# Optimization experiments

Hardware: AMD Instinct MI355X
Metric: run time of the kernel (lower is better)

Reference implementation:

```python
import jax, jax.numpy as jnp
import numpy as np
import itertools

DIM_X, DIM_Y = 3, 3
MAX_DIGIT = DIM_X * DIM_Y          # 9
NUM_NODES = MAX_DIGIT ** 2         # 81
EMBED = 16
HID = 96
BATCH = 256
ITERS = 4


def determine_edges(dim_x, dim_y):
    md = dim_x * dim_y
    rows = []
    for r in range(md):
        for c in range(md):
            s = {(r, i) for i in range(md)} | {(i, c) for i in range(md)}
            xm, ym = r // dim_x * dim_x, c // dim_y * dim_y
            s |= set(itertools.product(range(xm, xm + dim_x), range(ym, ym + dim_y)))
            s -= {(r, c)}
            rows.append(sorted(i * md + j for i, j in s))
    return np.asarray(rows, dtype=np.int32)  # [81, 20]


def mlp3(x, w0, b0, w1, b1, w2, b2):
    # MLP([a,b,c,d]): two ReLU hidden layers, linear output
    x = jax.nn.relu(x @ w0.T + b0)
    x = jax.nn.relu(x @ w1.T + b1)
    return x @ w2.T + b2


def setup_inputs() -> dict:
    key = jax.random.key(0)
    keys = iter(jax.random.split(key, 40))

    def lin(din, dout):
        kw, kb = jax.random.split(next(keys))
        lim = 1.0 / np.sqrt(din)
        w = jax.random.uniform(kw, (dout, din), jnp.float32, -lim, lim)
        b = jax.random.uniform(kb, (dout,), jnp.float32, -lim, lim)
        return w, b

    embed = jax.random.normal(next(keys), (MAX_DIGIT + 1, EMBED), jnp.float32)

    in_w0, in_b0 = lin(EMBED, HID); in_w1, in_b1 = lin(HID, HID); in_w2, in_b2 = lin(HID, HID)
    f_w0, f_b0 = lin(2 * HID, HID); f_w1, f_b1 = lin(HID, HID); f_w2, f_b2 = lin(HID, HID)
    g_w0, g_b0 = lin(2 * HID, HID); g_w1, g_b1 = lin(HID, HID); g_w2, g_b2 = lin(HID, HID)
    r_w0, r_b0 = lin(HID, HID); r_w1, r_b1 = lin(HID, HID); r_w2, r_b2 = lin(HID, MAX_DIGIT)

    lim = 1.0 / np.sqrt(HID)
    lstm_wih = jax.random.uniform(next(keys), (4 * HID, HID), jnp.float32, -lim, lim)
    lstm_whh = jax.random.uniform(next(keys), (4 * HID, HID), jnp.float32, -lim, lim)
    lstm_bih = jax.random.uniform(next(keys), (4 * HID,), jnp.float32, -lim, lim)
    lstm_bhh = jax.random.uniform(next(keys), (4 * HID,), jnp.float32, -lim, lim)

    grids = jax.random.randint(next(keys), (BATCH, NUM_NODES), 0, MAX_DIGIT + 1)
    c0 = jax.random.normal(next(keys), (BATCH * NUM_NODES, HID), jnp.float32)
    edges = jnp.asarray(determine_edges(DIM_X, DIM_Y))

    return dict(embed=embed,
                in_w0=in_w0, in_b0=in_b0, in_w1=in_w1, in_b1=in_b1, in_w2=in_w2, in_b2=in_b2,
                f_w0=f_w0, f_b0=f_b0, f_w1=f_w1, f_b1=f_b1, f_w2=f_w2, f_b2=f_b2,
                g_w0=g_w0, g_b0=g_b0, g_w1=g_w1, g_b1=g_b1, g_w2=g_w2, g_b2=g_b2,
                lstm_wih=lstm_wih, lstm_whh=lstm_whh, lstm_bih=lstm_bih, lstm_bhh=lstm_bhh,
                r_w0=r_w0, r_b0=r_b0, r_w1=r_w1, r_b1=r_b1, r_w2=r_w2, r_b2=r_b2,
                c0=c0, grids=grids, edges=edges, iters=ITERS)


def reference(embed,
              in_w0, in_b0, in_w1, in_b1, in_w2, in_b2,
              f_w0, f_b0, f_w1, f_b1, f_w2, f_b2,
              g_w0, g_b0, g_w1, g_b1, g_w2, g_b2,
              lstm_wih, lstm_whh, lstm_bih, lstm_bhh,
              r_w0, r_b0, r_w1, r_b1, r_w2, r_b2,
              c0, grids, edges, iters):
    B, N = grids.shape
    K = edges.shape[1]
    emb = embed[grids]                                   # [B, N, EMBED]
    X = mlp3(emb, in_w0, in_b0, in_w1, in_b1, in_w2, in_b2)  # [B, N, HID]
    H = X
    h = X.reshape(B * N, HID)
    c = c0
    outputs = []
    for _ in range(iters):
        # gather neighbor states: [B, N, K, HID]
        Hn = H[:, edges]
        Hs = jnp.broadcast_to(H[:, :, None, :], Hn.shape)
        pair = jnp.concatenate([Hs, Hn], axis=-1)        # [B, N, K, 2*HID]
        M = mlp3(pair, f_w0, f_b0, f_w1, f_b1, f_w2, f_b2).sum(axis=2)  # [B, N, HID]
        gin = mlp3(jnp.concatenate([X, M], axis=-1),
                   g_w0, g_b0, g_w1, g_b1, g_w2, g_b2).reshape(B * N, HID)
        # single-step LSTM (torch gate order: i, f, g, o)
        gates = gin @ lstm_wih.T + lstm_bih + h @ lstm_whh.T + lstm_bhh
        gi, gf, gg, go = jnp.split(gates, 4, axis=-1)
        c = jax.nn.sigmoid(gf) * c + jax.nn.sigmoid(gi) * jnp.tanh(gg)
        h = jax.nn.sigmoid(go) * jnp.tanh(c)
        H = h.reshape(B, N, HID)
        outputs.append(mlp3(H, r_w0, r_b0, r_w1, r_b1, r_w2, r_b2))  # [B, N, MAX_DIGIT]
    return jnp.stack(outputs)  # [iters, B, N, MAX_DIGIT]
```

## Files before the change

### kernel.cpp

```cpp
#include <hip/hip_runtime.h>
#include <hip/hip_bf16.h>

typedef __hip_bfloat16 bf16;
typedef __attribute__((ext_vector_type(8))) short short8;
typedef __attribute__((ext_vector_type(8))) __bf16 bf16x8;
typedef __attribute__((ext_vector_type(4))) float f32x4;

#define BN 20736
#define NNODE 81
#define KNB 20

__device__ inline float bf2f(short s) {
  union { unsigned u; float f; } x; x.u = ((unsigned)(unsigned short)s) << 16; return x.f;
}
__device__ inline short f2bf(float f) {
  __hip_bfloat16 h = __float2bfloat16(f);
  return *reinterpret_cast<short*>(&h);
}
__device__ inline bf16x8 ld8(const bf16* p) {
  return __builtin_bit_cast(bf16x8, *(const short8*)p);
}

__device__ inline void zacc3(f32x4 acc[3]) {
  #pragma unroll
  for (int nt = 0; nt < 3; ++nt) acc[nt] = (f32x4){0.f, 0.f, 0.f, 0.f};
}
__device__ inline void load_w48(const bf16* __restrict__ W, int ldw, int n0, int lr, int lq,
                                bf16x8 wf[3][3]) {
  #pragma unroll
  for (int nt = 0; nt < 3; ++nt)
    #pragma unroll
    for (int ks = 0; ks < 3; ++ks)
      wf[nt][ks] = ld8(&W[(size_t)(n0 + nt * 16 + lr) * ldw + ks * 32 + lq * 8]);
}
__device__ inline void gemm48(const bf16x8 af[3], const bf16x8 wf[3][3], f32x4 acc[3]) {
  #pragma unroll
  for (int ks = 0; ks < 3; ++ks)
    #pragma unroll
    for (int nt = 0; nt < 3; ++nt)
      acc[nt] = __builtin_amdgcn_mfma_f32_16x16x32_bf16(af[ks], wf[nt][ks], acc[nt], 0, 0, 0);
}
__device__ inline void acc_store_cs(float* xw, const f32x4 acc[3], int lr, int lq, int n0) {
  #pragma unroll
  for (int nt = 0; nt < 3; ++nt)
    #pragma unroll
    for (int r = 0; r < 4; ++r)
      xw[(lq * 4 + r) * 100 + n0 + nt * 16 + lr] = acc[nt][r];
}
__device__ inline void xbuf_frag(const float* xw, int lr, int lq,
                                 const float* __restrict__ bias, float bscale,
                                 const bf16* residRow, int act,
                                 bf16x8 af[3]) {
  #pragma unroll
  for (int ks = 0; ks < 3; ++ks) {
    const int c0 = ks * 32 + lq * 8;
    float4 x0 = *(const float4*)&xw[lr * 100 + c0];
    float4 x1 = *(const float4*)&xw[lr * 100 + c0 + 4];
    float xv[8] = {x0.x, x0.y, x0.z, x0.w, x1.x, x1.y, x1.z, x1.w};
    if (bias) {
      float4 b0 = *(const float4*)&bias[c0];
      float4 b1 = *(const float4*)&bias[c0 + 4];
      float bv[8] = {b0.x, b0.y, b0.z, b0.w, b1.x, b1.y, b1.z, b1.w};
      #pragma unroll
      for (int j = 0; j < 8; ++j) xv[j] += bscale * bv[j];
    }
    if (residRow) {
      short8 r8 = *(const short8*)&residRow[c0];
      #pragma unroll
      for (int j = 0; j < 8; ++j) xv[j] += bf2f(r8[j]);
    }
    short8 o;
    #pragma unroll
    for (int j = 0; j < 8; ++j) {
      float v = xv[j];
      if (act) v = fmaxf(v, 0.f);
      o[j] = f2bf(v);
    }
    af[ks] = __builtin_bit_cast(bf16x8, o);
  }
}
__device__ inline void store_frag(bf16* dst, int lq, const bf16x8 af[3]) {
  #pragma unroll
  for (int ks = 0; ks < 3; ++ks)
    *(short8*)&dst[ks * 32 + lq * 8] = __builtin_bit_cast(short8, af[ks]);
}

__global__ __launch_bounds__(256) void prep_k(
    const float* in_w1, const float* in_w2, const float* f_w1, const float* f_w2,
    const float* g_w1, const float* g_w2, const float* r_w0, const float* r_w1,
    const float* r_w2, const float* wih, const float* whh, const float* g_w0,
    const float* f_w0, const float* in_w0, const float* f_b0,
    bf16* inw1b, bf16* inw2b, bf16* fw1b, bf16* fw2b,
    bf16* gw1b, bf16* gw2b, bf16* rw0b, bf16* rw1b,
    bf16* rw2b, bf16* wihb, bf16* whhb, bf16* gw0b,
    bf16* wfnb, bf16* w0pb, float* bias_fn)
{
  int idx = blockIdx.x * 256 + threadIdx.x;
  int y = blockIdx.y;
  const float* src = nullptr; bf16* dst = nullptr; int cnt = 0;
  switch (y) {
    case 0:  src = in_w1; dst = inw1b; cnt = 9216;  break;
    case 1:  src = in_w2; dst = inw2b; cnt = 9216;  break;
    case 2:  src = f_w1;  dst = fw1b;  cnt = 9216;  break;
    case 3:  src = f_w2;  dst = fw2b;  cnt = 9216;  break;
    case 4:  src = g_w1;  dst = gw1b;  cnt = 9216;  break;
    case 5:  src = g_w2;  dst = gw2b;  cnt = 9216;  break;
    case 6:  src = r_w0;  dst = rw0b;  cnt = 9216;  break;
    case 7:  src = r_w1;  dst = rw1b;  cnt = 9216;  break;
    case 8:  src = r_w2;  dst = rw2b;  cnt = 864;   break;
    case 9:  src = wih;   dst = wihb;  cnt = 36864; break;
    case 10: src = whh;   dst = whhb;  cnt = 36864; break;
    case 11: src = g_w0;  dst = gw0b;  cnt = 18432; break;
    case 12: {
      if (idx < 18432) {
        int n = idx / 96, k = idx - n * 96;
        float v = (n < 96) ? f_w0[n * 192 + k] : f_w0[(n - 96) * 192 + 96 + k];
        wfnb[idx] = __float2bfloat16(v);
      }
      return;
    }
    case 13: {
      if (idx < 3072) {
        int n = idx >> 5, k = idx & 31;
        w0pb[idx] = __float2bfloat16(k < 16 ? in_w0[n * 16 + k] : 0.f);
      }
      return;
    }
    default: {
      if (idx < 192) bias_fn[idx] = (idx < 96) ? f_b0[idx] : 0.f;
      return;
    }
  }
  if (idx < cnt) dst[idx] = __float2bfloat16(src[idx]);
}

__global__ __launch_bounds__(256) void fused_in_k(
    const float* __restrict__ embed, const int* __restrict__ grids,
    const bf16* __restrict__ w0pb, const float* __restrict__ in_b0,
    const bf16* __restrict__ inw1b, const float* __restrict__ in_b1,
    const bf16* __restrict__ inw2b, const float* __restrict__ in_b2,
    const bf16* __restrict__ gw0b, const float* __restrict__ g_b0,
    const bf16* __restrict__ wfnb, const float* __restrict__ bias_fn,
    bf16* __restrict__ X, bf16* __restrict__ Xg, bf16* __restrict__ P)
{
  __shared__ float xbuf[2][2][1600];
  const int t = threadIdx.x, w = t >> 6, lane = t & 63, lr = lane & 15, lq = lane >> 4;
  const int mh = w >> 1, ch = w & 1, n0 = ch * 48;
  const int m0 = blockIdx.x * 32 + mh * 16;
  float* x0 = xbuf[0][mh];
  float* x1 = xbuf[1][mh];
  bf16x8 wf[3][3]; f32x4 acc[3]; bf16x8 af[3];

  short8 es = {0, 0, 0, 0, 0, 0, 0, 0};
  if (lq < 2) {
    int gidx = grids[m0 + lr];
    float4 e0 = *(const float4*)&embed[gidx * 16 + lq * 8];
    float4 e1 = *(const float4*)&embed[gidx * 16 + lq * 8 + 4];
    es[0] = f2bf(e0.x); es[1] = f2bf(e0.y); es[2] = f2bf(e0.z); es[3] = f2bf(e0.w);
    es[4] = f2bf(e1.x); es[5] = f2bf(e1.y); es[6] = f2bf(e1.z); es[7] = f2bf(e1.w);
  }
  bf16x8 a0 = __builtin_bit_cast(bf16x8, es);
  #pragma unroll
  for (int nt = 0; nt < 3; ++nt)
    wf[nt][0] = ld8(&w0pb[(size_t)(n0 + nt * 16 + lr) * 32 + lq * 8]);
  zacc3(acc);
  #pragma unroll
  for (int nt = 0; nt < 3; ++nt)
    acc[nt] = __builtin_amdgcn_mfma_f32_16x16x32_bf16(a0, wf[nt][0], acc[nt], 0, 0, 0);
  acc_store_cs(x0, acc, lr, lq, n0);
  __syncthreads();
  xbuf_frag(x0, lr, lq, in_b0, 1.f, nullptr, 1, af);
  load_w48(inw1b, 96, n0, lr, lq, wf); zacc3(acc); gemm48(af, wf, acc);
  acc_store_cs(x1, acc, lr, lq, n0);
  __syncthreads();
  xbuf_frag(x1, lr, lq, in_b1, 1.f, nullptr, 1, af);
  load_w48(inw2b, 96, n0, lr, lq, wf); zacc3(acc); gemm48(af, wf, acc);
  acc_store_cs(x0, acc, lr, lq, n0);
  __syncthreads();
  bf16x8 xf[3];
  xbuf_frag(x0, lr, lq, in_b2, 1.f, nullptr, 0, xf);
  if (ch == 0) store_frag(&X[(size_t)(m0 + lr) * 96], lq, xf);
  load_w48(gw0b, 192, n0, lr, lq, wf); zacc3(acc); gemm48(xf, wf, acc);
  acc_store_cs(x1, acc, lr, lq, n0);
  __syncthreads();
  xbuf_frag(x1, lr, lq, g_b0, 1.f, nullptr, 0, af);
  if (ch == 0) store_frag(&Xg[(size_t)(m0 + lr) * 96], lq, af);
  #pragma unroll
  for (int ph = 0; ph < 2; ++ph) {
    float* xb = ph ? x1 : x0;
    load_w48(wfnb + (size_t)ph * 96 * 96, 96, n0, lr, lq, wf); zacc3(acc); gemm48(xf, wf, acc);
    acc_store_cs(xb, acc, lr, lq, n0);
    __syncthreads();
    xbuf_frag(xb, lr, lq, bias_fn + ph * 96, 1.f, nullptr, 0, af);
    if (ch == 0) store_frag(&P[(size_t)(m0 + lr) * 192 + ph * 96], lq, af);
  }
}

__global__ __launch_bounds__(128) void edge_k(
    const bf16* __restrict__ P, const bf16* __restrict__ w1bf,
    const float* __restrict__ b1, const int* __restrict__ edges,
    const bf16* __restrict__ fw2b, const float* __restrict__ f_b2,
    bf16* __restrict__ M)
{
  __shared__ short zs[80 * 104];
  __shared__ short sbuf[16 * 104];
  const int t = threadIdx.x;
  const int grp = (blockIdx.x & 7) * 648 + (blockIdx.x >> 3);
  const int w = t >> 6, lane = t & 63, lr = lane & 15, lq = lane >> 4;
  const int n0 = w * 48;

  bf16x8 wf1[3][3];
  #pragma unroll
  for (int nt = 0; nt < 3; ++nt)
    #pragma unroll
    for (int ks = 0; ks < 3; ++ks)
      wf1[nt][ks] = ld8(&w1bf[(size_t)(n0 + nt * 16 + lr) * 96 + ks * 32 + lq * 8]);
  float b1v[3];
  #pragma unroll
  for (int nt = 0; nt < 3; ++nt) b1v[nt] = b1[n0 + nt * 16 + lr];

  for (int i = t; i < 12 * 104; i += 128) sbuf[(4 + i / 104) * 104 + (i % 104)] = 0;
  for (int cc = t; cc < 80 * 12; cc += 128) {
    int row = cc / 12, c8 = cc - row * 12;
    int p = row / 20, j = row - p * 20;
    int gr = grp * 4 + p;
    int b = gr / NNODE, i = gr - b * NNODE;
    int e = edges[i * KNB + j];
    short8 a8 = *(const short8*)&P[(size_t)gr * 192 + c8 * 8];
    short8 n8 = *(const short8*)&P[((size_t)b * NNODE + e) * 192 + 96 + c8 * 8];
    short8 z;
    #pragma unroll
    for (int q = 0; q < 8; ++q)
      z[q] = f2bf(fmaxf(bf2f(a8[q]) + bf2f(n8[q]), 0.f));
    *(short8*)&zs[row * 104 + c8 * 8] = z;
  }
  __syncthreads();

  f32x4 acc[5][3];
  #pragma unroll
  for (int mt = 0; mt < 5; ++mt)
    #pragma unroll
    for (int nt = 0; nt < 3; ++nt) acc[mt][nt] = (f32x4){0.f, 0.f, 0.f, 0.f};
  #pragma unroll
  for (int ks = 0; ks < 3; ++ks) {
    const int koff = ks * 32 + lq * 8;
    #pragma unroll
    for (int mt = 0; mt < 5; ++mt) {
      bf16x8 af = __builtin_bit_cast(bf16x8, *(const short8*)&zs[(mt * 16 + lr) * 104 + koff]);
      #pragma unroll
      for (int nt = 0; nt < 3; ++nt)
        acc[mt][nt] = __builtin_amdgcn_mfma_f32_16x16x32_bf16(af, wf1[nt][ks], acc[mt][nt], 0, 0, 0);
    }
  }

  float nodeacc[4][3];
  #pragma unroll
  for (int pp = 0; pp < 4; ++pp)
    #pragma unroll
    for (int nt = 0; nt < 3; ++nt) nodeacc[pp][nt] = 0.f;
  #pragma unroll
  for (int mt = 0; mt < 5; ++mt)
    #pragma unroll
    for (int nt = 0; nt < 3; ++nt)
      #pragma unroll
      for (int r = 0; r < 4; ++r) {
        int row = mt * 16 + lq * 4 + r;
        int p = row / 20;
        float v = fmaxf(acc[mt][nt][r] + b1v[nt], 0.f);
        #pragma unroll
        for (int pp = 0; pp < 4; ++pp)
          nodeacc[pp][nt] += (p == pp) ? v : 0.f;
      }
  #pragma unroll
  for (int pp = 0; pp < 4; ++pp)
    #pragma unroll
    for (int nt = 0; nt < 3; ++nt) {
      float v = nodeacc[pp][nt];
      v += __shfl_xor(v, 16, 64);
      v += __shfl_xor(v, 32, 64);
      if (lq == 0)
        sbuf[pp * 104 + n0 + nt * 16 + lr] = f2bf(v);
    }
  __syncthreads();

  bf16x8 mwf[3][3];
  #pragma unroll
  for (int nt = 0; nt < 3; ++nt)
    #pragma unroll
    for (int ks = 0; ks < 3; ++ks)
      mwf[nt][ks] = ld8(&fw2b[(size_t)(n0 + nt * 16 + lr) * 96 + ks * 32 + lq * 8]);
  f32x4 macc[3];
  zacc3(macc);
  #pragma unroll
  for (int ks = 0; ks < 3; ++ks) {
    bf16x8 af = __builtin_bit_cast(bf16x8, *(const short8*)&sbuf[lr * 104 + ks * 32 + lq * 8]);
    #pragma unroll
    for (int nt = 0; nt < 3; ++nt)
      macc[nt] = __builtin_amdgcn_mfma_f32_16x16x32_bf16(af, mwf[nt][ks], macc[nt], 0, 0, 0);
  }
  if (lq == 0) {
    #pragma unroll
    for (int nt = 0; nt < 3; ++nt) {
      int col = n0 + nt * 16 + lr;
      float bb = (float)KNB * f_b2[col];
      #pragma unroll
      for (int r = 0; r < 4; ++r)
        M[(size_t)(grp * 4 + r) * 96 + col] = __float2bfloat16(macc[nt][r] + bb);
    }
  }
}

__global__ __launch_bounds__(128) void fused_iter_k(
    const bf16* __restrict__ Min,
    const bf16* __restrict__ gw0b, const bf16* __restrict__ Xg,
    const bf16* __restrict__ gw1b, const float* __restrict__ g_b1,
    const bf16* __restrict__ gw2b, const float* __restrict__ g_b2,
    const bf16* __restrict__ Hin,
    const bf16* __restrict__ wihb, const bf16* __restrict__ whhb,
    const float* __restrict__ bih, const float* __restrict__ bhh,
    float* __restrict__ c, bf16* __restrict__ Hout,
    const bf16* __restrict__ wfnb, const float* __restrict__ bias_fn, bf16* __restrict__ P,
    const bf16* __restrict__ rw0b, const float* __restrict__ r_b0,
    const bf16* __restrict__ rw1b, const float* __restrict__ r_b1,
    const bf16* __restrict__ rw2b, const float* __restrict__ r_b2,
    float* __restrict__ outp, int doP)
{
  __shared__ float xb0[1600], xb1[1600];
  const int t = threadIdx.x, w = t >> 6, lane = t & 63, lr = lane & 15, lq = lane >> 4;
  const int n0 = w * 48;
  const int m0 = blockIdx.x * 16;

  bf16x8 wfA[3][3], wfB[3][3], af[3];
  f32x4 acc[3];

  #pragma unroll
  for (int ks = 0; ks < 3; ++ks)
    af[ks] = ld8(&Min[(size_t)(m0 + lr) * 96 + ks * 32 + lq * 8]);
  bf16x8 hin[3];
  #pragma unroll
  for (int ks = 0; ks < 3; ++ks)
    hin[ks] = ld8(&Hin[(size_t)(m0 + lr) * 96 + ks * 32 + lq * 8]);

  load_w48(gw0b + 96, 192, n0, lr, lq, wfA);
  zacc3(acc); gemm48(af, wfA, acc);
  load_w48(gw1b, 96, n0, lr, lq, wfB);
  acc_store_cs(xb0, acc, lr, lq, n0);
  __syncthreads();
  xbuf_frag(xb0, lr, lq, nullptr, 0.f, &Xg[(size_t)(m0 + lr) * 96], 1, af);
  zacc3(acc); gemm48(af, wfB, acc);
  load_w48(gw2b, 96, n0, lr, lq, wfA);
  acc_store_cs(xb1, acc, lr, lq, n0);
  __syncthreads();
  xbuf_frag(xb1, lr, lq, g_b1, 1.f, nullptr, 1, af);
  zacc3(acc); gemm48(af, wfA, acc);
  acc_store_cs(xb0, acc, lr, lq, n0);
  __syncthreads();
  bf16x8 gf[3];
  xbuf_frag(xb0, lr, lq, g_b2, 1.f, nullptr, 0, gf);

  float cv[3][4];
  #pragma unroll
  for (int nt = 0; nt < 3; ++nt)
    #pragma unroll
    for (int r = 0; r < 4; ++r)
      cv[nt][r] = c[(size_t)(m0 + lq * 4 + r) * 96 + n0 + nt * 16 + lr];

  f32x4 ga[4][3];
  #pragma unroll
  for (int g4 = 0; g4 < 4; ++g4)
    #pragma unroll
    for (int nt = 0; nt < 3; ++nt) ga[g4][nt] = (f32x4){0.f, 0.f, 0.f, 0.f};
  #pragma unroll
  for (int g4 = 0; g4 < 4; ++g4)
    #pragma unroll
    for (int nt = 0; nt < 3; ++nt) {
      size_t nrow = (size_t)(g4 * 96 + n0 + nt * 16 + lr) * 96;
      #pragma unroll
      for (int ks = 0; ks < 3; ++ks) {
        ga[g4][nt] = __builtin_amdgcn_mfma_f32_16x16x32_bf16(
            gf[ks], ld8(&wihb[nrow + ks * 32 + lq * 8]), ga[g4][nt], 0, 0, 0);
        ga[g4][nt] = __builtin_amdgcn_mfma_f32_16x16x32_bf16(
            hin[ks], ld8(&whhb[nrow + ks * 32 + lq * 8]), ga[g4][nt], 0, 0, 0);
      }
    }
  #pragma unroll
  for (int nt = 0; nt < 3; ++nt) {
    int col = n0 + nt * 16 + lr;
    float bvi = bih[col] + bhh[col];
    float bvf = bih[96 + col] + bhh[96 + col];
    float bvg = bih[192 + col] + bhh[192 + col];
    float bvo = bih[288 + col] + bhh[288 + col];
    #pragma unroll
    for (int r = 0; r < 4; ++r) {
      int m = m0 + lq * 4 + r;
      size_t idx = (size_t)m * 96 + col;
      float gi = ga[0][nt][r] + bvi;
      float gfv = ga[1][nt][r] + bvf;
      float gg = ga[2][nt][r] + bvg;
      float go = ga[3][nt][r] + bvo;
      float si = 1.f / (1.f + expf(-gi));
      float sf = 1.f / (1.f + expf(-gfv));
      float so = 1.f / (1.f + expf(-go));
      float tg = tanhf(gg);
      float cn = sf * cv[nt][r] + si * tg;
      if (doP) c[idx] = cn;
      xb1[(lq * 4 + r) * 100 + col] = so * tanhf(cn);
    }
  }
  __syncthreads();
  bf16x8 hf[3];
  xbuf_frag(xb1, lr, lq, nullptr, 0.f, nullptr, 0, hf);

  if (doP) {
    for (int cc = t; cc < 192; cc += 128) {
      int row = cc / 12, c8 = cc - row * 12;
      short8 o;
      #pragma unroll
      for (int j = 0; j < 8; ++j) o[j] = f2bf(xb1[row * 100 + c8 * 8 + j]);
      *(short8*)&Hout[(size_t)(m0 + row) * 96 + c8 * 8] = o;
    }
    load_w48(wfnb, 96, n0, lr, lq, wfA);
    zacc3(acc); gemm48(hf, wfA, acc);
    load_w48(wfnb + 96 * 96, 96, n0, lr, lq, wfB);
    #pragma unroll
    for (int nt = 0; nt < 3; ++nt) {
      float bvv = bias_fn[n0 + nt * 16 + lr];
      #pragma unroll
      for (int r = 0; r < 4; ++r)
        xb0[(lq * 4 + r) * 100 + n0 + nt * 16 + lr] = acc[nt][r] + bvv;
    }
    __syncthreads();
    for (int cc = t; cc < 192; cc += 128) {
      int row = cc / 12, c8 = cc - row * 12;
      short8 o;
      #pragma unroll
      for (int j = 0; j < 8; ++j) o[j] = f2bf(xb0[row * 100 + c8 * 8 + j]);
      *(short8*)&P[(size_t)(m0 + row) * 192 + c8 * 8] = o;
    }
    zacc3(acc); gemm48(hf, wfB, acc);
    #pragma unroll
    for (int nt = 0; nt < 3; ++nt) {
      float bvv = bias_fn[96 + n0 + nt * 16 + lr];
      #pragma unroll
      for (int r = 0; r < 4; ++r)
        xb1[(lq * 4 + r) * 100 + n0 + nt * 16 + lr] = acc[nt][r] + bvv;
    }
    __syncthreads();
    for (int cc = t; cc < 192; cc += 128) {
      int row = cc / 12, c8 = cc - row * 12;
      short8 o;
      #pragma unroll
      for (int j = 0; j < 8; ++j) o[j] = f2bf(xb1[row * 100 + c8 * 8 + j]);
      *(short8*)&P[(size_t)(m0 + row) * 192 + 96 + c8 * 8] = o;
    }
  }

  load_w48(rw0b, 96, n0, lr, lq, wfA);
  zacc3(acc); gemm48(hf, wfA, acc);
  load_w48(rw1b, 96, n0, lr, lq, wfB);
  __syncthreads();
  acc_store_cs(xb0, acc, lr, lq, n0);
  __syncthreads();
  xbuf_frag(xb0, lr, lq, r_b0, 1.f, nullptr, 1, af);
  zacc3(acc); gemm48(af, wfB, acc);
  acc_store_cs(xb1, acc, lr, lq, n0);
  __syncthreads();
  xbuf_frag(xb1, lr, lq, r_b1, 1.f, nullptr, 1, af);
  if (w == 0) {
    bf16x8 w9[3];
    #pragma unroll
    for (int ks = 0; ks < 3; ++ks) {
      short8 s = {0, 0, 0, 0, 0, 0, 0, 0};
      if (lr < 9) s = *(const short8*)&rw2b[(size_t)lr * 96 + ks * 32 + lq * 8];
      w9[ks] = __builtin_bit_cast(bf16x8, s);
    }
    f32x4 a9 = (f32x4){0.f, 0.f, 0.f, 0.f};
    #pragma unroll
    for (int ks = 0; ks < 3; ++ks)
      a9 = __builtin_amdgcn_mfma_f32_16x16x32_bf16(af[ks], w9[ks], a9, 0, 0, 0);
    if (lr < 9) {
      float bb = r_b2[lr];
      #pragma unroll
      for (int r = 0; r < 4; ++r)
        outp[(size_t)(m0 + lq * 4 + r) * 9 + lr] = a9[r] + bb;
    }
  }
}

extern "C" void kernel_launch(void* const* d_in, const int* in_sizes, int n_in,
                              void* d_out, int out_size, void* d_ws, size_t ws_size,
                              hipStream_t stream) {
  const float* embed   = (const float*)d_in[0];
  const float* in_w0   = (const float*)d_in[1];
  const float* in_b0   = (const float*)d_in[2];
  const float* in_w1   = (const float*)d_in[3];
  const float* in_b1   = (const float*)d_in[4];
  const float* in_w2   = (const float*)d_in[5];
  const float* in_b2   = (const float*)d_in[6];
  const float* f_w0    = (const float*)d_in[7];
  const float* f_b0    = (const float*)d_in[8];
  const float* f_w1    = (const float*)d_in[9];
  const float* f_b1    = (const float*)d_in[10];
  const float* f_w2    = (const float*)d_in[11];
  const float* f_b2    = (const float*)d_in[12];
  const float* g_w0    = (const float*)d_in[13];
  const float* g_b0    = (const float*)d_in[14];
  const float* g_w1    = (const float*)d_in[15];
  const float* g_b1    = (const float*)d_in[16];
  const float* g_w2    = (const float*)d_in[17];
  const float* g_b2    = (const float*)d_in[18];
  const float* wih     = (const float*)d_in[19];
  const float* whh     = (const float*)d_in[20];
  const float* bih     = (const float*)d_in[21];
  const float* bhh     = (const float*)d_in[22];
  const float* r_w0    = (const float*)d_in[23];
  const float* r_b0    = (const float*)d_in[24];
  const float* r_w1    = (const float*)d_in[25];
  const float* r_b1    = (const float*)d_in[26];
  const float* r_w2    = (const float*)d_in[27];
  const float* r_b2    = (const float*)d_in[28];
  const float* c0      = (const float*)d_in[29];
  const int*   grids   = (const int*)d_in[30];
  const int*   edges   = (const int*)d_in[31];

  float* out = (float*)d_out;
  const int iters = out_size / (BN * 9);

  float* c    = (float*)d_ws;
  bf16* H0    = (bf16*)(c + (size_t)BN * 96);
  bf16* H1    = H0 + (size_t)BN * 96;
  bf16* Xg    = H1 + (size_t)BN * 96;
  bf16* P     = Xg + (size_t)BN * 96;
  bf16* Mb    = P  + (size_t)BN * 192;
  bf16* w0pb  = Mb + (size_t)BN * 96;
  bf16* wfnb  = w0pb + 3072;
  bf16* inw1b = wfnb + 18432;
  bf16* inw2b = inw1b + 9216;
  bf16* fw1b  = inw2b + 9216;
  bf16* fw2b  = fw1b + 9216;
  bf16* gw0b  = fw2b + 9216;
  bf16* gw1b  = gw0b + 18432;
  bf16* gw2b  = gw1b + 9216;
  bf16* rw0b  = gw2b + 9216;
  bf16* rw1b  = rw0b + 9216;
  bf16* rw2b  = rw1b + 9216;
  bf16* wihb  = rw2b + 864;
  bf16* whhb  = wihb + 36864;
  float* bias_fn = (float*)(whhb + 36864);

  prep_k<<<dim3(144, 15), 256, 0, stream>>>(
      in_w1, in_w2, f_w1, f_w2, g_w1, g_w2, r_w0, r_w1, r_w2, wih, whh, g_w0,
      f_w0, in_w0, f_b0,
      inw1b, inw2b, fw1b, fw2b, gw1b, gw2b, rw0b, rw1b, rw2b, wihb, whhb, gw0b,
      wfnb, w0pb, bias_fn);
  fused_in_k<<<BN / 32, 256, 0, stream>>>(embed, grids, w0pb, in_b0, inw1b, in_b1,
                                          inw2b, in_b2, gw0b, g_b0, wfnb, bias_fn,
                                          H0, Xg, P);
  hipMemcpyAsync(c, c0, (size_t)BN * 96 * sizeof(float), hipMemcpyDeviceToDevice, stream);

  for (int it = 0; it < iters; ++it) {
    bf16* Hin  = (it & 1) ? H1 : H0;
    bf16* Hout = (it & 1) ? H0 : H1;
    edge_k<<<BN / 4, 128, 0, stream>>>(P, fw1b, f_b1, edges, fw2b, f_b2, Mb);
    fused_iter_k<<<BN / 16, 128, 0, stream>>>(
        Mb, gw0b, Xg, gw1b, g_b1, gw2b, g_b2,
        Hin, wihb, whhb, bih, bhh, c, Hout,
        wfnb, bias_fn, P, rw0b, r_b0, rw1b, r_b1, rw2b, r_b2,
        out + (size_t)it * BN * 9, it < iters - 1 ? 1 : 0);
  }
}
```

Baseline: 327.6 us.

## Run fused_iter_k with one wavefront per block covering all 96 columns

The per-node iteration kernel now uses a single 64-lane wave per 16-row tile instead of two waves each owning 48 output columns. Each wave computes all 96 columns, with weight fragments streamed straight from global memory inside a new gemm96w helper. This lets every __syncthreads be dropped, since LDS staging is now private to one wave. The trade-off is twice the accumulator registers per wave (the LSTM gate accumulators grow to 4x6 tiles), which may cost occupancy or cause spills, and weights are no longer preloaded ahead of each GEMM.

```diff
diff --git a/kernel.cpp b/kernel.cpp
--- a/kernel.cpp
+++ b/kernel.cpp
@@ -46,6 +46,27 @@
     #pragma unroll
     for (int r = 0; r < 4; ++r)
       xw[(lq * 4 + r) * 100 + n0 + nt * 16 + lr] = acc[nt][r];
+}
+__device__ inline void zacc6(f32x4 acc[6]) {
+  #pragma unroll
+  for (int nt = 0; nt < 6; ++nt) acc[nt] = (f32x4){0.f, 0.f, 0.f, 0.f};
+}
+__device__ inline void gemm96w(const bf16* __restrict__ W, int ldw,
+                               const bf16x8 af[3], int lr, int lq, f32x4 acc[6]) {
+  #pragma unroll
+  for (int nt = 0; nt < 6; ++nt)
+    #pragma unroll
+    for (int ks = 0; ks < 3; ++ks) {
+      bf16x8 wf = ld8(&W[(size_t)(nt * 16 + lr) * ldw + ks * 32 + lq * 8]);
+      acc[nt] = __builtin_amdgcn_mfma_f32_16x16x32_bf16(af[ks], wf, acc[nt], 0, 0, 0);
+    }
+}
+__device__ inline void acc_store96(float* xw, const f32x4 acc[6], int lr, int lq) {
+  #pragma unroll
+  for (int nt = 0; nt < 6; ++nt)
+    #pragma unroll
+    for (int r = 0; r < 4; ++r)
+      xw[(lq * 4 + r) * 100 + nt * 16 + lr] = acc[nt][r];
 }
 __device__ inline void xbuf_frag(const float* xw, int lr, int lq,
                                  const float* __restrict__ bias, float bscale,
@@ -310,7 +331,7 @@
   }
 }
 
-__global__ __launch_bounds__(128) void fused_iter_k(
+__global__ __launch_bounds__(64) void fused_iter_k(
     const bf16* __restrict__ Min,
     const bf16* __restrict__ gw0b, const bf16* __restrict__ Xg,
     const bf16* __restrict__ gw1b, const float* __restrict__ g_b1,
@@ -326,12 +347,11 @@
     float* __restrict__ outp, int doP)
 {
   __shared__ float xb0[1600], xb1[1600];
-  const int t = threadIdx.x, w = t >> 6, lane = t & 63, lr = lane & 15, lq = lane >> 4;
-  const int n0 = w * 48;
+  const int t = threadIdx.x, lr = t & 15, lq = t >> 4;
   const int m0 = blockIdx.x * 16;
 
-  bf16x8 wfA[3][3], wfB[3][3], af[3];
-  f32x4 acc[3];
+  bf16x8 af[3];
+  f32x4 acc[6];
 
   #pragma unroll
   for (int ks = 0; ks < 3; ++ks)
@@ -341,40 +361,34 @@
   for (int ks = 0; ks < 3; ++ks)
     hin[ks] = ld8(&Hin[(size_t)(m0 + lr) * 96 + ks * 32 + lq * 8]);
 
-  load_w48(gw0b + 96, 192, n0, lr, lq, wfA);
-  zacc3(acc); gemm48(af, wfA, acc);
-  load_w48(gw1b, 96, n0, lr, lq, wfB);
-  acc_store_cs(xb0, acc, lr, lq, n0);
-  __syncthreads();
+  zacc6(acc); gemm96w(gw0b + 96, 192, af, lr, lq, acc);
+  acc_store96(xb0, acc, lr, lq);
   xbuf_frag(xb0, lr, lq, nullptr, 0.f, &Xg[(size_t)(m0 + lr) * 96], 1, af);
-  zacc3(acc); gemm48(af, wfB, acc);
-  load_w48(gw2b, 96, n0, lr, lq, wfA);
-  acc_store_cs(xb1, acc, lr, lq, n0);
-  __syncthreads();
+  zacc6(acc); gemm96w(gw1b, 96, af, lr, lq, acc);
+  acc_store96(xb1, acc, lr, lq);
   xbuf_frag(xb1, lr, lq, g_b1, 1.f, nullptr, 1, af);
-  zacc3(acc); gemm48(af, wfA, acc);
-  acc_store_cs(xb0, acc, lr, lq, n0);
-  __syncthreads();
+  zacc6(acc); gemm96w(gw2b, 96, af, lr, lq, acc);
+  acc_store96(xb0, acc, lr, lq);
   bf16x8 gf[3];
   xbuf_frag(xb0, lr, lq, g_b2, 1.f, nullptr, 0, gf);
 
-  float cv[3][4];
-  #pragma unroll
-  for (int nt = 0; nt < 3; ++nt)
+  float cv[6][4];
+  #pragma unroll
+  for (int nt = 0; nt < 6; ++nt)
     #pragma unroll
     for (int r = 0; r < 4; ++r)
-      cv[nt][r] = c[(size_t)(m0 + lq * 4 + r) * 96 + n0 + nt * 16 + lr];
-
-  f32x4 ga[4][3];
+      cv[nt][r] = c[(size_t)(m0 + lq * 4 + r) * 96 + nt * 16 + lr];
+
+  f32x4 ga[4][6];
   #pragma unroll
   for (int g4 = 0; g4 < 4; ++g4)
     #pragma unroll
-    for (int nt = 0; nt < 3; ++nt) ga[g4][nt] = (f32x4){0.f, 0.f, 0.f, 0.f};
+    for (int nt = 0; nt < 6; ++nt) ga[g4][nt] = (f32x4){0.f, 0.f, 0.f, 0.f};
   #pragma unroll
   for (int g4 = 0; g4 < 4; ++g4)
     #pragma unroll
-    for (int nt = 0; nt < 3; ++nt) {
-      size_t nrow = (size_t)(g4 * 96 + n0 + nt * 16 + lr) * 96;
+    for (int nt = 0; nt < 6; ++nt) {
+      size_t nrow = (size_t)(g4 * 96 + nt * 16 + lr) * 96;
       #pragma unroll
       for (int ks = 0; ks < 3; ++ks) {
         ga[g4][nt] = __builtin_amdgcn_mfma_f32_16x16x32_bf16(
@@ -384,8 +398,8 @@
       }
     }
   #pragma unroll
-  for (int nt = 0; nt < 3; ++nt) {
-    int col = n0 + nt * 16 + lr;
+  for (int nt = 0; nt < 6; ++nt) {
+    int col = nt * 16 + lr;
     float bvi = bih[col] + bhh[col];
     float bvf = bih[96 + col] + bhh[96 + col];
     float bvg = bih[192 + col] + bhh[192 + col];
@@ -407,47 +421,48 @@
       xb1[(lq * 4 + r) * 100 + col] = so * tanhf(cn);
     }
   }
-  __syncthreads();
   bf16x8 hf[3];
   xbuf_frag(xb1, lr, lq, nullptr, 0.f, nullptr, 0, hf);
 
   if (doP) {
-    for (int cc = t; cc < 192; cc += 128) {
-      int row = cc / 12, c8 = cc - row * 12;
+    #pragma unroll
+    for (int cc = 0; cc < 3; ++cc) {
+      int idx = t + cc * 64;
+      int row = idx / 12, c8 = idx - row * 12;
       short8 o;
       #pragma unroll
       for (int j = 0; j < 8; ++j) o[j] = f2bf(xb1[row * 100 + c8 * 8 + j]);
       *(short8*)&Hout[(size_t)(m0 + row) * 96 + c8 * 8] = o;
     }
-    load_w48(wfnb, 96, n0, lr, lq, wfA);
-    zacc3(acc); gemm48(hf, wfA, acc);
-    load_w48(wfnb + 96 * 96, 96, n0, lr, lq, wfB);
-    #pragma unroll
-    for (int nt = 0; nt < 3; ++nt) {
-      float bvv = bias_fn[n0 + nt * 16 + lr];
+    zacc6(acc); gemm96w(wfnb, 96, hf, lr, lq, acc);
+    #pragma unroll
+    for (int nt = 0; nt < 6; ++nt) {
+      float bvv = bias_fn[nt * 16 + lr];
       #pragma unroll
       for (int r = 0; r < 4; ++r)
-        xb0[(lq * 4 + r) * 100 + n0 + nt * 16 + lr] = acc[nt][r] + bvv;
-    }
-    __syncthreads();
-    for (int cc = t; cc < 192; cc += 128) {
-      int row = cc / 12, c8 = cc - row * 12;
+        xb0[(lq * 4 + r) * 100 + nt * 16 + lr] = acc[nt][r] + bvv;
+    }
+    #pragma unroll
+    for (int cc = 0; cc < 3; ++cc) {
+      int idx = t + cc * 64;
+      int row = idx / 12, c8 = idx - row * 12;
       short8 o;
       #pragma unroll
       for (int j = 0; j < 8; ++j) o[j] = f2bf(xb0[row * 100 + c8 * 8 + j]);
       *(short8*)&P[(size_t)(m0 + row) * 192 + c8 * 8] = o;
     }
-    zacc3(acc); gemm48(hf, wfB, acc);
-    #pragma unroll
-    for (int nt = 0; nt < 3; ++nt) {
-      float bvv = bias_fn[96 + n0 + nt * 16 + lr];
+    zacc6(acc); gemm96w(wfnb + 96 * 96, 96, hf, lr, lq, acc);
+    #pragma unroll
+    for (int nt = 0; nt < 6; ++nt) {
+      float bvv = bias_fn[96 + nt * 16 + lr];
       #pragma unroll
       for (int r = 0; r < 4; ++r)
-        xb1[(lq * 4 + r) * 100 + n0 + nt * 16 + lr] = acc[nt][r] + bvv;
-    }
-    __syncthreads();
-    for (int cc = t; cc < 192; cc += 128) {
-      int row = cc / 12, c8 = cc - row * 12;
+        xb1[(lq * 4 + r) * 100 + nt * 16 + lr] = acc[nt][r] + bvv;
+    }
+    #pragma unroll
+    for (int cc = 0; cc < 3; ++cc) {
+      int idx = t + cc * 64;
+      int row = idx / 12, c8 = idx - row * 12;
       short8 o;
       #pragma unroll
       for (int j = 0; j < 8; ++j) o[j] = f2bf(xb1[row * 100 + c8 * 8 + j]);
@@ -455,18 +470,13 @@
     }
   }
 
-  load_w48(rw0b, 96, n0, lr, lq, wfA);
-  zacc3(acc); gemm48(hf, wfA, acc);
-  load_w48(rw1b, 96, n0, lr, lq, wfB);
-  __syncthreads();
-  acc_store_cs(xb0, acc, lr, lq, n0);
-  __syncthreads();
+  zacc6(acc); gemm96w(rw0b, 96, hf, lr, lq, acc);
+  acc_store96(xb0, acc, lr, lq);
   xbuf_frag(xb0, lr, lq, r_b0, 1.f, nullptr, 1, af);
-  zacc3(acc); gemm48(af, wfB, acc);
-  acc_store_cs(xb1, acc, lr, lq, n0);
-  __syncthreads();
+  zacc6(acc); gemm96w(rw1b, 96, af, lr, lq, acc);
+  acc_store96(xb1, acc, lr, lq);
   xbuf_frag(xb1, lr, lq, r_b1, 1.f, nullptr, 1, af);
-  if (w == 0) {
+  {
     bf16x8 w9[3];
     #pragma unroll
     for (int ks = 0; ks < 3; ++ks) {
@@ -562,7 +572,7 @@
     bf16* Hin  = (it & 1) ? H1 : H0;
     bf16* Hout = (it & 1) ? H0 : H1;
     edge_k<<<BN / 4, 128, 0, stream>>>(P, fw1b, f_b1, edges, fw2b, f_b2, Mb);
-    fused_iter_k<<<BN / 16, 128, 0, stream>>>(
+    fused_iter_k<<<BN / 16, 64, 0, stream>>>(
         Mb, gw0b, Xg, gw1b, g_b1, gw2b, g_b2,
         Hin, wihb, whhb, bih, bhh, c, Hout,
         wfnb, bias_fn, P, rw0b, r_b0, rw1b, r_b1, rw2b, r_b2,
```

After: 343.2 us. 1.05x slower.

## Fold linear layers into precomputed combined weights for message and LSTM input

Applied to the files above, without the earlier changes.

Because the last layer of the f MLP and of the g MLP are linear with no activation, their weights are multiplied into the next linear layer once on the device: g_w0's message half times f_w2, and wih times g_w2, with the biases folded to match. This removes the per-node f_w2 GEMM and its shared-memory round trip from the edge kernel, and removes one 96x96 GEMM stage plus a barrier from the iteration kernel. The cost is a small extra prep kernel that runs serial dot products per output element, and some bf16 rounding differences from using the combined weights.

```diff
diff --git a/kernel.cpp b/kernel.cpp
--- a/kernel.cpp
+++ b/kernel.cpp
@@ -134,6 +134,39 @@
   if (idx < cnt) dst[idx] = __float2bfloat16(src[idx]);
 }
 
+__global__ __launch_bounds__(256) void prep2_k(
+    const float* __restrict__ g_w0, const float* __restrict__ f_w2,
+    const float* __restrict__ f_b2, const float* __restrict__ wih,
+    const float* __restrict__ g_w2, const float* __restrict__ g_b2,
+    const float* __restrict__ bih, const float* __restrict__ bhh,
+    bf16* __restrict__ wmcb, float* __restrict__ b_mc,
+    bf16* __restrict__ wgcb, float* __restrict__ b_lc)
+{
+  int idx = blockIdx.x * 256 + threadIdx.x;
+  if (idx < 9216) {
+    int n = idx / 96, k = idx - n * 96;
+    float s = 0.f;
+    for (int j = 0; j < 96; ++j) s += g_w0[n * 192 + 96 + j] * f_w2[j * 96 + k];
+    wmcb[idx] = __float2bfloat16(s);
+  } else if (idx < 9216 + 36864) {
+    int r = idx - 9216;
+    int m = r / 96, k = r - m * 96;
+    float s = 0.f;
+    for (int j = 0; j < 96; ++j) s += wih[m * 96 + j] * g_w2[j * 96 + k];
+    wgcb[r] = __float2bfloat16(s);
+  } else if (idx < 9216 + 36864 + 96) {
+    int n = idx - 9216 - 36864;
+    float s = 0.f;
+    for (int j = 0; j < 96; ++j) s += g_w0[n * 192 + 96 + j] * 20.f * f_b2[j];
+    b_mc[n] = s;
+  } else if (idx < 9216 + 36864 + 96 + 384) {
+    int m = idx - 9216 - 36864 - 96;
+    float s = bih[m] + bhh[m];
+    for (int j = 0; j < 96; ++j) s += wih[m * 96 + j] * g_b2[j];
+    b_lc[m] = s;
+  }
+}
+
 __global__ __launch_bounds__(256) void fused_in_k(
     const float* __restrict__ embed, const int* __restrict__ grids,
     const bf16* __restrict__ w0pb, const float* __restrict__ in_b0,
@@ -199,11 +232,9 @@
 __global__ __launch_bounds__(128) void edge_k(
     const bf16* __restrict__ P, const bf16* __restrict__ w1bf,
     const float* __restrict__ b1, const int* __restrict__ edges,
-    const bf16* __restrict__ fw2b, const float* __restrict__ f_b2,
-    bf16* __restrict__ M)
+    bf16* __restrict__ S)
 {
   __shared__ short zs[80 * 104];
-  __shared__ short sbuf[16 * 104];
   const int t = threadIdx.x;
   const int grp = (blockIdx.x & 7) * 648 + (blockIdx.x >> 3);
   const int w = t >> 6, lane = t & 63, lr = lane & 15, lq = lane >> 4;
@@ -219,7 +250,6 @@
   #pragma unroll
   for (int nt = 0; nt < 3; ++nt) b1v[nt] = b1[n0 + nt * 16 + lr];
 
-  for (int i = t; i < 12 * 104; i += 128) sbuf[(4 + i / 104) * 104 + (i % 104)] = 0;
   for (int cc = t; cc < 80 * 12; cc += 128) {
     int row = cc / 12, c8 = cc - row * 12;
     int p = row / 20, j = row - p * 20;
@@ -279,45 +309,18 @@
       v += __shfl_xor(v, 16, 64);
       v += __shfl_xor(v, 32, 64);
       if (lq == 0)
-        sbuf[pp * 104 + n0 + nt * 16 + lr] = f2bf(v);
-    }
-  __syncthreads();
-
-  bf16x8 mwf[3][3];
-  #pragma unroll
-  for (int nt = 0; nt < 3; ++nt)
-    #pragma unroll
-    for (int ks = 0; ks < 3; ++ks)
-      mwf[nt][ks] = ld8(&fw2b[(size_t)(n0 + nt * 16 + lr) * 96 + ks * 32 + lq * 8]);
-  f32x4 macc[3];
-  zacc3(macc);
-  #pragma unroll
-  for (int ks = 0; ks < 3; ++ks) {
-    bf16x8 af = __builtin_bit_cast(bf16x8, *(const short8*)&sbuf[lr * 104 + ks * 32 + lq * 8]);
-    #pragma unroll
-    for (int nt = 0; nt < 3; ++nt)
-      macc[nt] = __builtin_amdgcn_mfma_f32_16x16x32_bf16(af, mwf[nt][ks], macc[nt], 0, 0, 0);
-  }
-  if (lq == 0) {
-    #pragma unroll
-    for (int nt = 0; nt < 3; ++nt) {
-      int col = n0 + nt * 16 + lr;
-      float bb = (float)KNB * f_b2[col];
-      #pragma unroll
-      for (int r = 0; r < 4; ++r)
-        M[(size_t)(grp * 4 + r) * 96 + col] = __float2bfloat16(macc[nt][r] + bb);
-    }
-  }
+        S[(size_t)(grp * 4 + pp) * 96 + n0 + nt * 16 + lr] = __float2bfloat16(v);
+    }
 }
 
 __global__ __launch_bounds__(128) void fused_iter_k(
-    const bf16* __restrict__ Min,
-    const bf16* __restrict__ gw0b, const bf16* __restrict__ Xg,
+    const bf16* __restrict__ Sin,
+    const bf16* __restrict__ wmcb, const float* __restrict__ b_mc,
+    const bf16* __restrict__ Xg,
     const bf16* __restrict__ gw1b, const float* __restrict__ g_b1,
-    const bf16* __restrict__ gw2b, const float* __restrict__ g_b2,
     const bf16* __restrict__ Hin,
-    const bf16* __restrict__ wihb, const bf16* __restrict__ whhb,
-    const float* __restrict__ bih, const float* __restrict__ bhh,
+    const bf16* __restrict__ wgcb, const bf16* __restrict__ whhb,
+    const float* __restrict__ b_lc,
     float* __restrict__ c, bf16* __restrict__ Hout,
     const bf16* __restrict__ wfnb, const float* __restrict__ bias_fn, bf16* __restrict__ P,
     const bf16* __restrict__ rw0b, const float* __restrict__ r_b0,
@@ -335,28 +338,23 @@
 
   #pragma unroll
   for (int ks = 0; ks < 3; ++ks)
-    af[ks] = ld8(&Min[(size_t)(m0 + lr) * 96 + ks * 32 + lq * 8]);
+    af[ks] = ld8(&Sin[(size_t)(m0 + lr) * 96 + ks * 32 + lq * 8]);
   bf16x8 hin[3];
   #pragma unroll
   for (int ks = 0; ks < 3; ++ks)
     hin[ks] = ld8(&Hin[(size_t)(m0 + lr) * 96 + ks * 32 + lq * 8]);
 
-  load_w48(gw0b + 96, 192, n0, lr, lq, wfA);
+  load_w48(wmcb, 96, n0, lr, lq, wfA);
   zacc3(acc); gemm48(af, wfA, acc);
   load_w48(gw1b, 96, n0, lr, lq, wfB);
   acc_store_cs(xb0, acc, lr, lq, n0);
   __syncthreads();
-  xbuf_frag(xb0, lr, lq, nullptr, 0.f, &Xg[(size_t)(m0 + lr) * 96], 1, af);
+  xbuf_frag(xb0, lr, lq, b_mc, 1.f, &Xg[(size_t)(m0 + lr) * 96], 1, af);
   zacc3(acc); gemm48(af, wfB, acc);
-  load_w48(gw2b, 96, n0, lr, lq, wfA);
   acc_store_cs(xb1, acc, lr, lq, n0);
   __syncthreads();
-  xbuf_frag(xb1, lr, lq, g_b1, 1.f, nullptr, 1, af);
-  zacc3(acc); gemm48(af, wfA, acc);
-  acc_store_cs(xb0, acc, lr, lq, n0);
-  __syncthreads();
-  bf16x8 gf[3];
-  xbuf_frag(xb0, lr, lq, g_b2, 1.f, nullptr, 0, gf);
+  bf16x8 zf[3];
+  xbuf_frag(xb1, lr, lq, g_b1, 1.f, nullptr, 1, zf);
 
   float cv[3][4];
   #pragma unroll
@@ -378,7 +376,7 @@
       #pragma unroll
       for (int ks = 0; ks < 3; ++ks) {
         ga[g4][nt] = __builtin_amdgcn_mfma_f32_16x16x32_bf16(
-            gf[ks], ld8(&wihb[nrow + ks * 32 + lq * 8]), ga[g4][nt], 0, 0, 0);
+            zf[ks], ld8(&wgcb[nrow + ks * 32 + lq * 8]), ga[g4][nt], 0, 0, 0);
         ga[g4][nt] = __builtin_amdgcn_mfma_f32_16x16x32_bf16(
             hin[ks], ld8(&whhb[nrow + ks * 32 + lq * 8]), ga[g4][nt], 0, 0, 0);
       }
@@ -386,10 +384,10 @@
   #pragma unroll
   for (int nt = 0; nt < 3; ++nt) {
     int col = n0 + nt * 16 + lr;
-    float bvi = bih[col] + bhh[col];
-    float bvf = bih[96 + col] + bhh[96 + col];
-    float bvg = bih[192 + col] + bhh[192 + col];
-    float bvo = bih[288 + col] + bhh[288 + col];
+    float bvi = b_lc[col];
+    float bvf = b_lc[96 + col];
+    float bvg = b_lc[192 + col];
+    float bvo = b_lc[288 + col];
     #pragma unroll
     for (int r = 0; r < 4; ++r) {
       int m = m0 + lq * 4 + r;
@@ -531,8 +529,8 @@
   bf16* H1    = H0 + (size_t)BN * 96;
   bf16* Xg    = H1 + (size_t)BN * 96;
   bf16* P     = Xg + (size_t)BN * 96;
-  bf16* Mb    = P  + (size_t)BN * 192;
-  bf16* w0pb  = Mb + (size_t)BN * 96;
+  bf16* Sb    = P  + (size_t)BN * 192;
+  bf16* w0pb  = Sb + (size_t)BN * 96;
   bf16* wfnb  = w0pb + 3072;
   bf16* inw1b = wfnb + 18432;
   bf16* inw2b = inw1b + 9216;
@@ -546,13 +544,19 @@
   bf16* rw2b  = rw1b + 9216;
   bf16* wihb  = rw2b + 864;
   bf16* whhb  = wihb + 36864;
-  float* bias_fn = (float*)(whhb + 36864);
+  bf16* wmcb  = whhb + 36864;
+  bf16* wgcb  = wmcb + 9216;
+  float* bias_fn = (float*)(wgcb + 36864);
+  float* b_mc    = bias_fn + 192;
+  float* b_lc    = b_mc + 96;
 
   prep_k<<<dim3(144, 15), 256, 0, stream>>>(
       in_w1, in_w2, f_w1, f_w2, g_w1, g_w2, r_w0, r_w1, r_w2, wih, whh, g_w0,
       f_w0, in_w0, f_b0,
       inw1b, inw2b, fw1b, fw2b, gw1b, gw2b, rw0b, rw1b, rw2b, wihb, whhb, gw0b,
       wfnb, w0pb, bias_fn);
+  prep2_k<<<(9216 + 36864 + 480 + 255) / 256, 256, 0, stream>>>(
+      g_w0, f_w2, f_b2, wih, g_w2, g_b2, bih, bhh, wmcb, b_mc, wgcb, b_lc);
   fused_in_k<<<BN / 32, 256, 0, stream>>>(embed, grids, w0pb, in_b0, inw1b, in_b1,
                                           inw2b, in_b2, gw0b, g_b0, wfnb, bias_fn,
                                           H0, Xg, P);
@@ -561,10 +565,10 @@
   for (int it = 0; it < iters; ++it) {
     bf16* Hin  = (it & 1) ? H1 : H0;
     bf16* Hout = (it & 1) ? H0 : H1;
-    edge_k<<<BN / 4, 128, 0, stream>>>(P, fw1b, f_b1, edges, fw2b, f_b2, Mb);
+    edge_k<<<BN / 4, 128, 0, stream>>>(P, fw1b, f_b1, edges, Sb);
     fused_iter_k<<<BN / 16, 128, 0, stream>>>(
-        Mb, gw0b, Xg, gw1b, g_b1, gw2b, g_b2,
-        Hin, wihb, whhb, bih, bhh, c, Hout,
+        Sb, wmcb, b_mc, Xg, gw1b, g_b1,
+        Hin, wgcb, whhb, b_lc, c, Hout,
         wfnb, bias_fn, P, rw0b, r_b0, rw1b, r_b1, rw2b, r_b2,
         out + (size_t)it * BN * 9, it < iters - 1 ? 1 : 0);
   }
```

Measured after the change: 316.6 us. -3.3%, faster.
